# Performance work log

Measured on AMD Instinct MI355X. Metric: run time of the kernel, lower is better.

## Reference

```python
import math
import jax, jax.numpy as jnp
import numpy as np

B, L, D_IN, H, NLAYER, FUT, MDIM = 16, 128, 8, 128, 2, 12, 2

def setup_inputs() -> dict:
    key = jax.random.key(0)
    ks = jax.random.split(key, 16)
    def rn(k, shape, scale=0.05):
        return jax.random.normal(k, shape, jnp.float32) * scale
    return {
        'history': jax.random.normal(ks[0], (B, L, D_IN), jnp.float32),
        'history_mask': jnp.ones((B, L), jnp.float32),
        'Wp': rn(ks[1], (D_IN, H)), 'bp': jnp.zeros((H,), jnp.float32),
        'We1': rn(ks[2], (NLAYER, 4, H)), 'be1': jnp.zeros((NLAYER, H), jnp.float32),
        'We2': rn(ks[3], (NLAYER, H, H)), 'be2': jnp.zeros((NLAYER, H), jnp.float32),
        'Wa1': rn(ks[4], (NLAYER, 3 * H, H)), 'ba1': jnp.zeros((NLAYER, H), jnp.float32),
        'wa2': rn(ks[5], (NLAYER, H)), 'ba2': jnp.zeros((NLAYER,), jnp.float32),
        'Wm1': rn(ks[6], (NLAYER, 2 * H, H)), 'bm1': jnp.zeros((NLAYER, H), jnp.float32),
        'Wm2': rn(ks[7], (NLAYER, H, H)), 'bm2': jnp.zeros((NLAYER, H), jnp.float32),
        'Wo1': rn(ks[8], (NLAYER, 2 * H, H)), 'bo1': jnp.zeros((NLAYER, H), jnp.float32),
        'Wo2': rn(ks[9], (NLAYER, H, H)), 'bo2': jnp.zeros((NLAYER, H), jnp.float32),
        'ln_g': jnp.ones((NLAYER, H), jnp.float32), 'ln_b': jnp.zeros((NLAYER, H), jnp.float32),
        'hg': jnp.ones((D_IN + H,), jnp.float32), 'hb': jnp.zeros((D_IN + H,), jnp.float32),
        'Wh1': rn(ks[10], (D_IN + H, H)), 'bh1': jnp.zeros((H,), jnp.float32),
        'Wh2': rn(ks[11], (H, FUT * MDIM)), 'bh2': jnp.zeros((FUT * MDIM,), jnp.float32),
    }

def _layer_norm(x, g, b):
    mu = jnp.mean(x, -1, keepdims=True)
    var = jnp.mean((x - mu) ** 2, -1, keepdims=True)
    return (x - mu) * jax.lax.rsqrt(var + 1e-5) * g + b

def _forward(history, history_mask, Wp, bp, We1, be1, We2, be2, Wa1, ba1, wa2, ba2,
             Wm1, bm1, Wm2, bm2, Wo1, bo1, Wo2, bo2, ln_g, ln_b, hg, hb, Wh1, bh1, Wh2, bh2):
    valid = history_mask > 0
    vm = valid.astype(jnp.float32)[..., None]
    ts = jnp.cumsum(jnp.maximum(history[..., 5], 0.0), axis=1)
    # edge features [B,L,L,4]: dist, dt/300, same_src, same_step
    lat, lon, src_flag = history[..., 0], history[..., 1], history[..., 6]
    dlat = lat[:, :, None] - lat[:, None, :]
    dlon = lon[:, :, None] - lon[:, None, :]
    dist = jnp.sqrt(dlat * dlat + dlon * dlon + 1e-8)
    dt = jnp.abs(ts[:, :, None] - ts[:, None, :]) / 300.0
    same_src = (src_flag[:, :, None] == src_flag[:, None, :]).astype(jnp.float32)
    same_step = jnp.broadcast_to(jnp.eye(L, dtype=jnp.float32), (B, L, L))
    edge_feat = jnp.stack([dist, dt, same_src, same_step], axis=-1)
    h = (history @ Wp + bp) * vm
    inv = 1.0 / math.sqrt(H)
    for l in range(NLAYER):
        eh = jax.nn.relu(edge_feat @ We1[l] + be1[l]) @ We2[l] + be2[l]  # [B,L,L,H]
        # att MLP on concat([src,dst,edge]) -> split first weight into blocks
        sa = h @ Wa1[l, :H]       # src term, varies over i
        da = h @ Wa1[l, H:2 * H]  # dst term, varies over j
        att_hid = jnp.tanh(sa[:, :, None, :] + da[:, None, :, :] + eh @ Wa1[l, 2 * H:] + ba1[l])
        att = (att_hid @ wa2[l] + ba2[l]) * inv  # [B,L,L]
        att = jnp.where(valid[:, None, :], att, -1e9)  # key invalid
        att = jnp.where(valid[:, :, None], att, -1e9)  # query invalid
        w = jax.nn.softmax(att, axis=-1)
        # msg MLP on concat([src, edge])
        msg = jax.nn.relu((h @ Wm1[l, :H])[:, :, None, :] + eh @ Wm1[l, H:] + bm1[l]) @ Wm2[l] + bm2[l]
        agg = jnp.einsum('bij,bijk->bik', w, msg)
        out = jax.nn.relu(h @ Wo1[l, :H] + agg @ Wo1[l, H:] + bo1[l]) @ Wo2[l] + bo2[l]
        h = _layer_norm(h + out, ln_g[l], ln_b[l]) * vm
    # decoder state: last valid step
    vc = jnp.clip(jnp.sum(history_mask, axis=1).astype(jnp.int32), 1, L)
    last = vc - 1
    bidx = jnp.arange(B)
    ds = jnp.concatenate([history[bidx, last], h[bidx, last]], axis=-1)
    x = _layer_norm(ds, hg, hb)
    pred = (jax.nn.relu(x @ Wh1 + bh1) @ Wh2 + bh2).reshape(B, FUT, MDIM)
    pred = jnp.nan_to_num(pred, nan=0.0, posinf=1e4, neginf=-1e4)
    return pred, h

def reference(history, history_mask, Wp, bp, We1, be1, We2, be2, Wa1, ba1, wa2, ba2,
              Wm1, bm1, Wm2, bm2, Wo1, bo1, Wo2, bo2, ln_g, ln_b, hg, hb, Wh1, bh1, Wh2, bh2):
    return _forward(history, history_mask, Wp, bp, We1, be1, We2, be2, Wa1, ba1, wa2, ba2,
                    Wm1, bm1, Wm2, bm2, Wo1, bo1, Wo2, bo2, ln_g, ln_b, hg, hb, Wh1, bh1, Wh2, bh2)
```

## Files before the change

kernel.cpp:

```cpp
#include <hip/hip_runtime.h>
#include <math.h>

#define BB 16
#define LL 128
#define D_IN 8
#define HH 128
#define NLAYER 2
#define FUT 12
#define MDIM 2

typedef __attribute__((ext_vector_type(8))) __bf16 bf16x8;
typedef __attribute__((ext_vector_type(8))) short short8v;
typedef __attribute__((ext_vector_type(4))) float f32x4;

#define MFMA_B16(A, B, C) __builtin_amdgcn_mfma_f32_16x16x32_bf16(A, B, C, 0, 0, 0)

static __device__ __forceinline__ short f2bf(float f) {
    union { float f; unsigned u; } v; v.f = f;
    unsigned r = v.u + 0x7FFFu + ((v.u >> 16) & 1u);
    return (short)(r >> 16);
}

static __device__ __forceinline__ float tanh_fast(float x) {
    float e = __expf(2.f * x);
    return 1.f - 2.f / (e + 1.f);
}

__global__ __launch_bounds__(LL) void k_ts(const float* __restrict__ hist, float* __restrict__ ts) {
    int b = blockIdx.x, j = threadIdx.x;
    __shared__ float s[LL];
    s[j] = fmaxf(hist[(b * LL + j) * D_IN + 5], 0.f);
    __syncthreads();
    for (int d = 1; d < LL; d <<= 1) {
        float add = (j >= d) ? s[j - d] : 0.f;
        __syncthreads();
        s[j] += add;
        __syncthreads();
    }
    ts[b * LL + j] = s[j];
}

__global__ __launch_bounds__(256) void k_h0(const float* __restrict__ hist, const float* __restrict__ mask,
                                            const float* __restrict__ Wp, const float* __restrict__ bp,
                                            float* __restrict__ h) {
    int idx = blockIdx.x * 256 + threadIdx.x;
    if (idx >= BB * LL * HH) return;
    int k = idx & (HH - 1);
    int bi = idx >> 7;
    const float* hr = hist + (size_t)bi * D_IN;
    float acc = bp[k];
#pragma unroll
    for (int f = 0; f < D_IN; f++) acc += hr[f] * Wp[f * HH + k];
    float vm = mask[bi] > 0.f ? 1.f : 0.f;
    h[idx] = acc * vm;
}

__global__ __launch_bounds__(HH) void k_compose(const float* __restrict__ We2, const float* __restrict__ be2,
                                                const float* __restrict__ Wa1, const float* __restrict__ ba1,
                                                const float* __restrict__ Wm1, const float* __restrict__ bm1,
                                                short* __restrict__ AmT, short* __restrict__ MmT,
                                                float* __restrict__ ca, float* __restrict__ cm) {
    int blk = blockIdx.x;
    int l = blk / (HH + 1);
    int p = blk % (HH + 1);
    int q = threadIdx.x;
    __shared__ float row[HH];
    const float* WaE = Wa1 + (size_t)(l * 3 * HH + 2 * HH) * HH;
    const float* WmE = Wm1 + (size_t)(l * 2 * HH + HH) * HH;
    if (p < HH) {
        row[q] = We2[(size_t)(l * HH + p) * HH + q];
        __syncthreads();
        float a = 0.f, m = 0.f;
        for (int k = 0; k < HH; k++) { float w = row[k]; a += w * WaE[k * HH + q]; m += w * WmE[k * HH + q]; }
        AmT[(size_t)l * HH * HH + q * HH + p] = f2bf(a);
        MmT[(size_t)l * HH * HH + q * HH + p] = f2bf(m);
    } else {
        row[q] = be2[l * HH + q];
        __syncthreads();
        float a = 0.f, m = 0.f;
        for (int k = 0; k < HH; k++) { float w = row[k]; a += w * WaE[k * HH + q]; m += w * WmE[k * HH + q]; }
        ca[l * HH + q] = a + ba1[l * HH + q];
        cm[l * HH + q] = m + bm1[l * HH + q];
    }
}

__global__ __launch_bounds__(256) void k_wconv(const float* __restrict__ Wa1, const float* __restrict__ Wm1,
                                               const float* __restrict__ Wo1, const float* __restrict__ Wm2,
                                               const float* __restrict__ Wo2,
                                               short* __restrict__ WT4, short* __restrict__ WT3) {
    int blk = blockIdx.x;
    int l = blk / 7, m = blk % 7;
    const float* src;
    switch (m) {
        case 0: src = Wa1 + (size_t)(l * 3 * HH) * HH; break;
        case 1: src = Wa1 + (size_t)(l * 3 * HH + HH) * HH; break;
        case 2: src = Wm1 + (size_t)(l * 2 * HH) * HH; break;
        case 3: src = Wo1 + (size_t)(l * 2 * HH) * HH; break;
        case 4: src = Wm2 + (size_t)l * HH * HH; break;
        case 5: src = Wo1 + (size_t)(l * 2 * HH + HH) * HH; break;
        default: src = Wo2 + (size_t)l * HH * HH; break;
    }
    short* dst = (m < 4) ? (WT4 + (size_t)(l * 4 + m) * HH * HH) : (WT3 + (size_t)(l * 3 + (m - 4)) * HH * HH);
    int tid = threadIdx.x;
#pragma unroll 4
    for (int e = 0; e < 64; e++) {
        int idx = e * 256 + tid;
        int c = idx >> 7, k = idx & (HH - 1);
        dst[c * HH + k] = f2bf(src[k * HH + c]);
    }
}

__global__ __launch_bounds__(256) void k_pre(const float* __restrict__ h, const short* __restrict__ WT4,
                                             const float* __restrict__ ca, const float* __restrict__ cm,
                                             float* __restrict__ base_a, float* __restrict__ da,
                                             float* __restrict__ base_m, float* __restrict__ oa, int l) {
    __shared__ __align__(16) short hA[32][136];
    const int tid = threadIdx.x, lane = tid & 63, wv = tid >> 6;
    const int lo = lane & 15, g4 = lane >> 4;
    const int r0 = blockIdx.x * 32;
    {
        int row = tid >> 3, cc = (tid & 7) * 16;
        const float* hr = h + (size_t)(r0 + row) * HH + cc;
        short8v pk;
#pragma unroll
        for (int e = 0; e < 8; e++) pk[e] = f2bf(hr[e]);
        *(short8v*)&hA[row][cc] = pk;
#pragma unroll
        for (int e = 0; e < 8; e++) pk[e] = f2bf(hr[8 + e]);
        *(short8v*)&hA[row][cc + 8] = pk;
    }
    __syncthreads();
    bf16x8 af[2][4];
#pragma unroll
    for (int mt = 0; mt < 2; mt++)
#pragma unroll
        for (int ks = 0; ks < 4; ks++)
            af[mt][ks] = *(const bf16x8*)&hA[mt * 16 + lo][ks * 32 + g4 * 8];
    const short* Wl = WT4 + (size_t)(l * 4 + wv) * HH * HH;
    float* dst;
    const float* bias = nullptr;
    if (wv == 0) { dst = base_a; bias = ca + l * HH; }
    else if (wv == 1) dst = da;
    else if (wv == 2) { dst = base_m; bias = cm + l * HH; }
    else dst = oa;
#pragma unroll
    for (int ct = 0; ct < 8; ct++) {
        int col = ct * 16 + lo;
        bf16x8 Bf[4];
#pragma unroll
        for (int ks = 0; ks < 4; ks++)
            Bf[ks] = *(const bf16x8*)(Wl + (size_t)col * HH + ks * 32 + g4 * 8);
        f32x4 acc[2];
        acc[0] = (f32x4){0.f, 0.f, 0.f, 0.f};
        acc[1] = (f32x4){0.f, 0.f, 0.f, 0.f};
#pragma unroll
        for (int ks = 0; ks < 4; ks++) {
            acc[0] = MFMA_B16(af[0][ks], Bf[ks], acc[0]);
            acc[1] = MFMA_B16(af[1][ks], Bf[ks], acc[1]);
        }
        float bv = bias ? bias[col] : 0.f;
#pragma unroll
        for (int mt = 0; mt < 2; mt++)
#pragma unroll
            for (int rg = 0; rg < 4; rg++)
                dst[(size_t)(r0 + mt * 16 + g4 * 4 + rg) * HH + col] = acc[mt][rg] + bv;
    }
}

__global__ __launch_bounds__(256, 4) void k_attn(
    const float* __restrict__ hist, const float* __restrict__ mask, const float* __restrict__ ts,
    const float* __restrict__ base_a_g, const float* __restrict__ base_m_g, const float* __restrict__ da,
    const short* __restrict__ AmT, const short* __restrict__ MmT,
    const float* __restrict__ wa2, const float* __restrict__ ba2,
    const float* __restrict__ We1, const float* __restrict__ be1,
    float* __restrict__ v_out, int l) {
    __shared__ __align__(16) short t_lds[LL][136];
    __shared__ float bufA[512];
    __shared__ float bufB[128];
    __shared__ float val_s[128], base_a[128], base_m[128], wa2_s[128];

    const int tid = threadIdx.x;
    const int lane = tid & 63;
    const int wv = tid >> 6;
    const int lo = lane & 15, g4 = lane >> 4;
    const int bi = blockIdx.x, b = bi >> 7, i = bi & (LL - 1);

    bf16x8 Bf[2][4];
#pragma unroll
    for (int ct = 0; ct < 2; ct++) {
        int col = wv * 32 + ct * 16 + lo;
#pragma unroll
        for (int ks = 0; ks < 4; ks++)
            Bf[ct][ks] = *(const bf16x8*)(AmT + (size_t)l * HH * HH + col * HH + ks * 32 + g4 * 8);
    }

    const float* We1l = We1 + l * 4 * HH;
    bufA[tid] = We1l[tid];
    bufA[tid + 256] = We1l[tid + 256];
    if (tid < LL) {
        val_s[tid] = mask[b * LL + tid];
        wa2_s[tid] = wa2[l * HH + tid];
        bufB[tid] = be1[l * HH + tid];
        base_a[tid] = base_a_g[(size_t)bi * HH + tid];
        base_m[tid] = base_m_g[(size_t)bi * HH + tid];
    }
    __syncthreads();

    {
        int jj = tid & (LL - 1);
        const float* hri = hist + (size_t)(b * LL + i) * D_IN;
        const float* hrj = hist + (size_t)(b * LL + jj) * D_IN;
        float dlat = hri[0] - hrj[0], dlon = hri[1] - hrj[1];
        float ea = sqrtf(dlat * dlat + dlon * dlon + 1e-8f);
        float eb = fabsf(ts[b * LL + i] - ts[b * LL + jj]) * (1.f / 300.f);
        float ec = (hri[6] == hrj[6]) ? 1.f : 0.f;
        float ed = (jj == i) ? 1.f : 0.f;
#pragma unroll
        for (int pass = 0; pass < 8; pass++) {
            int r0 = ((tid >> 7) + pass * 2) * 8;
            short8v pk;
#pragma unroll
            for (int e = 0; e < 8; e++) {
                int r = r0 + e;
                float v = ea * bufA[r] + eb * bufA[128 + r] + ec * bufA[256 + r] + ed * bufA[384 + r] + bufB[r];
                pk[e] = f2bf(fmaxf(v, 0.f));
            }
            *(short8v*)&t_lds[jj][r0] = pk;
        }
    }

    f32x4 acc[8][2];
    const float* da_b = da + (size_t)(b * LL) * HH;
#pragma unroll
    for (int jt = 0; jt < 8; jt++)
#pragma unroll
        for (int ct = 0; ct < 2; ct++)
#pragma unroll
            for (int rg = 0; rg < 4; rg++)
                acc[jt][ct][rg] = da_b[(size_t)(jt * 16 + g4 * 4 + rg) * HH + wv * 32 + ct * 16 + lo];
    __syncthreads();

#pragma unroll
    for (int ks = 0; ks < 4; ks++) {
#pragma unroll
        for (int jh = 0; jh < 2; jh++) {
            bf16x8 tf[4];
#pragma unroll
            for (int m = 0; m < 4; m++)
                tf[m] = *(const bf16x8*)&t_lds[(jh * 4 + m) * 16 + lo][ks * 32 + g4 * 8];
#pragma unroll
            for (int m = 0; m < 4; m++) {
                acc[jh * 4 + m][0] = MFMA_B16(tf[m], Bf[0][ks], acc[jh * 4 + m][0]);
                acc[jh * 4 + m][1] = MFMA_B16(tf[m], Bf[1][ks], acc[jh * 4 + m][1]);
            }
        }
    }

#pragma unroll
    for (int ct = 0; ct < 2; ct++) {
        int col = wv * 32 + ct * 16 + lo;
#pragma unroll
        for (int ks = 0; ks < 4; ks++)
            Bf[ct][ks] = *(const bf16x8*)(MmT + (size_t)l * HH * HH + col * HH + ks * 32 + g4 * 8);
    }

    {
        int k0 = wv * 32 + lo, k1 = k0 + 16;
        float ba0 = base_a[k0], ba1v = base_a[k1];
        float w0a = wa2_s[k0], w1a = wa2_s[k1];
#pragma unroll
        for (int jt = 0; jt < 8; jt++) {
#pragma unroll
            for (int rg = 0; rg < 4; rg++) {
                float p = tanh_fast(acc[jt][0][rg] + ba0) * w0a + tanh_fast(acc[jt][1][rg] + ba1v) * w1a;
                p += __shfl_xor(p, 1);
                p += __shfl_xor(p, 2);
                p += __shfl_xor(p, 4);
                p += __shfl_xor(p, 8);
                if (lo == 0) bufA[wv * LL + jt * 16 + g4 * 4 + rg] = p;
            }
        }
    }
    __syncthreads();

    float w0, w1;
    {
        const float inv = 0.08838834764831845f;
        float ba2l = ba2[l];
        float vi = val_s[i];
        float a0 = (bufA[lane] + bufA[128 + lane] + bufA[256 + lane] + bufA[384 + lane] + ba2l) * inv;
        float a1 = (bufA[64 + lane] + bufA[192 + lane] + bufA[320 + lane] + bufA[448 + lane] + ba2l) * inv;
        if (!(val_s[lane] > 0.f) || !(vi > 0.f)) a0 = -1e9f;
        if (!(val_s[64 + lane] > 0.f) || !(vi > 0.f)) a1 = -1e9f;
        float m = fmaxf(a0, a1);
#pragma unroll
        for (int d = 1; d < 64; d <<= 1) m = fmaxf(m, __shfl_xor(m, d));
        float e0 = __expf(a0 - m), e1 = __expf(a1 - m);
        float s = e0 + e1;
#pragma unroll
        for (int d = 1; d < 64; d <<= 1) s += __shfl_xor(s, d);
        float rs = 1.f / s;
        w0 = e0 * rs;
        w1 = e1 * rs;
    }

#pragma unroll
    for (int jt = 0; jt < 8; jt++)
#pragma unroll
        for (int ct = 0; ct < 2; ct++)
#pragma unroll
            for (int rg = 0; rg < 4; rg++) acc[jt][ct][rg] = 0.f;
#pragma unroll
    for (int ks = 0; ks < 4; ks++) {
#pragma unroll
        for (int jh = 0; jh < 2; jh++) {
            bf16x8 tf[4];
#pragma unroll
            for (int m = 0; m < 4; m++)
                tf[m] = *(const bf16x8*)&t_lds[(jh * 4 + m) * 16 + lo][ks * 32 + g4 * 8];
#pragma unroll
            for (int m = 0; m < 4; m++) {
                acc[jh * 4 + m][0] = MFMA_B16(tf[m], Bf[0][ks], acc[jh * 4 + m][0]);
                acc[jh * 4 + m][1] = MFMA_B16(tf[m], Bf[1][ks], acc[jh * 4 + m][1]);
            }
        }
    }

    {
        int k0 = wv * 32 + lo;
        float bm0 = base_m[k0], bm1v = base_m[k0 + 16];
        float mac0 = 0.f, mac1 = 0.f;
#pragma unroll
        for (int jt = 0; jt < 8; jt++) {
#pragma unroll
            for (int rg = 0; rg < 4; rg++) {
                int j = jt * 16 + g4 * 4 + rg;
                float wj = (jt < 4) ? __shfl(w0, j) : __shfl(w1, j - 64);
                mac0 += wj * fmaxf(acc[jt][0][rg] + bm0, 0.f);
                mac1 += wj * fmaxf(acc[jt][1][rg] + bm1v, 0.f);
            }
        }
        mac0 += __shfl_xor(mac0, 16);
        mac0 += __shfl_xor(mac0, 32);
        mac1 += __shfl_xor(mac1, 16);
        mac1 += __shfl_xor(mac1, 32);
        if (g4 == 0) {
            v_out[(size_t)bi * HH + wv * 32 + lo] = mac0;
            v_out[(size_t)bi * HH + wv * 32 + 16 + lo] = mac1;
        }
    }
}

__global__ __launch_bounds__(256) void k_post(
    const float* __restrict__ v, const float* __restrict__ oa, const float* __restrict__ h,
    const float* __restrict__ mask, const short* __restrict__ WT3,
    const float* __restrict__ bm2, const float* __restrict__ bo1, const float* __restrict__ bo2,
    const float* __restrict__ ln_g, const float* __restrict__ ln_b,
    float* __restrict__ hout, float* __restrict__ hcopy, int l) {
    __shared__ __align__(16) short xA[32][136];
    __shared__ __align__(16) short iA[32][136];
    __shared__ float red[2][4][32];
    const int tid = threadIdx.x, lane = tid & 63, wv = tid >> 6;
    const int lo = lane & 15, g4 = lane >> 4;
    const int r0 = blockIdx.x * 32;

    float oaR[2][2][4], hR[2][2][4], vmR[2][4];
    float bm2R[2], bo1R[2], bo2R[2], gR[2], bR[2];
#pragma unroll
    for (int ct = 0; ct < 2; ct++) {
        int c = wv * 32 + ct * 16 + lo;
        bm2R[ct] = bm2[l * HH + c];
        bo1R[ct] = bo1[l * HH + c];
        bo2R[ct] = bo2[l * HH + c];
        gR[ct] = ln_g[l * HH + c];
        bR[ct] = ln_b[l * HH + c];
    }
#pragma unroll
    for (int mt = 0; mt < 2; mt++)
#pragma unroll
        for (int rg = 0; rg < 4; rg++) {
            int r = r0 + mt * 16 + g4 * 4 + rg;
            vmR[mt][rg] = mask[r];
#pragma unroll
            for (int ct = 0; ct < 2; ct++) {
                int c = wv * 32 + ct * 16 + lo;
                oaR[mt][ct][rg] = oa[(size_t)r * HH + c];
                hR[mt][ct][rg] = h[(size_t)r * HH + c];
            }
        }

    {
        int row = tid >> 3, cc = (tid & 7) * 16;
        const float* vr = v + (size_t)(r0 + row) * HH + cc;
        short8v pk;
#pragma unroll
        for (int e = 0; e < 8; e++) pk[e] = f2bf(vr[e]);
        *(short8v*)&xA[row][cc] = pk;
#pragma unroll
        for (int e = 0; e < 8; e++) pk[e] = f2bf(vr[8 + e]);
        *(short8v*)&xA[row][cc + 8] = pk;
    }
    __syncthreads();

    bf16x8 af[2][4], Bf[2][4];
    f32x4 acc[2][2];

    {
        const short* W = WT3 + (size_t)(l * 3 + 0) * HH * HH;
#pragma unroll
        for (int mt = 0; mt < 2; mt++)
#pragma unroll
            for (int ks = 0; ks < 4; ks++)
                af[mt][ks] = *(const bf16x8*)&xA[mt * 16 + lo][ks * 32 + g4 * 8];
#pragma unroll
        for (int ct = 0; ct < 2; ct++) {
            int col = wv * 32 + ct * 16 + lo;
#pragma unroll
            for (int ks = 0; ks < 4; ks++)
                Bf[ct][ks] = *(const bf16x8*)(W + (size_t)col * HH + ks * 32 + g4 * 8);
        }
#pragma unroll
        for (int mt = 0; mt < 2; mt++)
#pragma unroll
            for (int ct = 0; ct < 2; ct++) acc[mt][ct] = (f32x4){0.f, 0.f, 0.f, 0.f};
#pragma unroll
        for (int ks = 0; ks < 4; ks++)
#pragma unroll
            for (int mt = 0; mt < 2; mt++) {
                acc[mt][0] = MFMA_B16(af[mt][ks], Bf[0][ks], acc[mt][0]);
                acc[mt][1] = MFMA_B16(af[mt][ks], Bf[1][ks], acc[mt][1]);
            }
#pragma unroll
        for (int mt = 0; mt < 2; mt++)
#pragma unroll
            for (int ct = 0; ct < 2; ct++)
#pragma unroll
                for (int rg = 0; rg < 4; rg++)
                    iA[mt * 16 + g4 * 4 + rg][wv * 32 + ct * 16 + lo] = f2bf(acc[mt][ct][rg] + bm2R[ct]);
    }
    __syncthreads();

    {
        const short* W = WT3 + (size_t)(l * 3 + 1) * HH * HH;
#pragma unroll
        for (int mt = 0; mt < 2; mt++)
#pragma unroll
            for (int ks = 0; ks < 4; ks++)
                af[mt][ks] = *(const bf16x8*)&iA[mt * 16 + lo][ks * 32 + g4 * 8];
#pragma unroll
        for (int ct = 0; ct < 2; ct++) {
            int col = wv * 32 + ct * 16 + lo;
#pragma unroll
            for (int ks = 0; ks < 4; ks++)
                Bf[ct][ks] = *(const bf16x8*)(W + (size_t)col * HH + ks * 32 + g4 * 8);
        }
#pragma unroll
        for (int mt = 0; mt < 2; mt++)
#pragma unroll
            for (int ct = 0; ct < 2; ct++) acc[mt][ct] = (f32x4){0.f, 0.f, 0.f, 0.f};
#pragma unroll
        for (int ks = 0; ks < 4; ks++)
#pragma unroll
            for (int mt = 0; mt < 2; mt++) {
                acc[mt][0] = MFMA_B16(af[mt][ks], Bf[0][ks], acc[mt][0]);
                acc[mt][1] = MFMA_B16(af[mt][ks], Bf[1][ks], acc[mt][1]);
            }
#pragma unroll
        for (int mt = 0; mt < 2; mt++)
#pragma unroll
            for (int ct = 0; ct < 2; ct++)
#pragma unroll
                for (int rg = 0; rg < 4; rg++)
                    xA[mt * 16 + g4 * 4 + rg][wv * 32 + ct * 16 + lo] =
                        f2bf(fmaxf(acc[mt][ct][rg] + oaR[mt][ct][rg] + bo1R[ct], 0.f));
    }
    __syncthreads();

    float y[2][2][4];
    {
        const short* W = WT3 + (size_t)(l * 3 + 2) * HH * HH;
#pragma unroll
        for (int mt = 0; mt < 2; mt++)
#pragma unroll
            for (int ks = 0; ks < 4; ks++)
                af[mt][ks] = *(const bf16x8*)&xA[mt * 16 + lo][ks * 32 + g4 * 8];
#pragma unroll
        for (int ct = 0; ct < 2; ct++) {
            int col = wv * 32 + ct * 16 + lo;
#pragma unroll
            for (int ks = 0; ks < 4; ks++)
                Bf[ct][ks] = *(const bf16x8*)(W + (size_t)col * HH + ks * 32 + g4 * 8);
        }
#pragma unroll
        for (int mt = 0; mt < 2; mt++)
#pragma unroll
            for (int ct = 0; ct < 2; ct++) acc[mt][ct] = (f32x4){0.f, 0.f, 0.f, 0.f};
#pragma unroll
        for (int ks = 0; ks < 4; ks++)
#pragma unroll
            for (int mt = 0; mt < 2; mt++) {
                acc[mt][0] = MFMA_B16(af[mt][ks], Bf[0][ks], acc[mt][0]);
                acc[mt][1] = MFMA_B16(af[mt][ks], Bf[1][ks], acc[mt][1]);
            }
#pragma unroll
        for (int mt = 0; mt < 2; mt++)
#pragma unroll
            for (int ct = 0; ct < 2; ct++)
#pragma unroll
                for (int rg = 0; rg < 4; rg++)
                    y[mt][ct][rg] = acc[mt][ct][rg] + bo2R[ct] + hR[mt][ct][rg];
    }
#pragma unroll
    for (int mt = 0; mt < 2; mt++)
#pragma unroll
        for (int rg = 0; rg < 4; rg++) {
            float s = y[mt][0][rg] + y[mt][1][rg];
            float s2 = y[mt][0][rg] * y[mt][0][rg] + y[mt][1][rg] * y[mt][1][rg];
#pragma unroll
            for (int d = 1; d < 16; d <<= 1) { s += __shfl_xor(s, d); s2 += __shfl_xor(s2, d); }
            if (lo == 0) {
                red[0][wv][mt * 16 + g4 * 4 + rg] = s;
                red[1][wv][mt * 16 + g4 * 4 + rg] = s2;
            }
        }
    __syncthreads();
#pragma unroll
    for (int mt = 0; mt < 2; mt++)
#pragma unroll
        for (int rg = 0; rg < 4; rg++) {
            int rl = mt * 16 + g4 * 4 + rg;
            float mu = (red[0][0][rl] + red[0][1][rl] + red[0][2][rl] + red[0][3][rl]) * (1.f / HH);
            float ex2 = (red[1][0][rl] + red[1][1][rl] + red[1][2][rl] + red[1][3][rl]) * (1.f / HH);
            float var = ex2 - mu * mu;
            float rs = rsqrtf(var + 1e-5f);
            float vm = vmR[mt][rg] > 0.f ? 1.f : 0.f;
            int r = r0 + rl;
#pragma unroll
            for (int ct = 0; ct < 2; ct++) {
                int c = wv * 32 + ct * 16 + lo;
                float hv = ((y[mt][ct][rg] - mu) * rs * gR[ct] + bR[ct]) * vm;
                hout[(size_t)r * HH + c] = hv;
                if (hcopy) hcopy[(size_t)r * HH + c] = hv;
            }
        }
}

__global__ __launch_bounds__(HH) void k_dec(const float* __restrict__ hist, const float* __restrict__ mask,
                                            const float* __restrict__ h, const float* __restrict__ hg,
                                            const float* __restrict__ hb, const float* __restrict__ Wh1,
                                            const float* __restrict__ bh1, const float* __restrict__ Wh2,
                                            const float* __restrict__ bh2, float* __restrict__ out) {
    int b = blockIdx.x, t = threadIdx.x;
    const int N = D_IN + HH;
    __shared__ float red[HH], x_s[D_IN + HH], u_s[HH];
    red[t] = mask[b * LL + t];
    __syncthreads();
    for (int s = 64; s > 0; s >>= 1) { if (t < s) red[t] += red[t + s]; __syncthreads(); }
    int vc = (int)red[0];
    vc = min(max(vc, 1), LL);
    int last = vc - 1;
    __syncthreads();
    if (t < D_IN) x_s[t] = hist[(size_t)(b * LL + last) * D_IN + t];
    x_s[D_IN + t] = h[(size_t)(b * LL + last) * HH + t];
    __syncthreads();
    float ps = 0.f;
    for (int f = t; f < N; f += HH) ps += x_s[f];
    red[t] = ps;
    __syncthreads();
    for (int s = 64; s > 0; s >>= 1) { if (t < s) red[t] += red[t + s]; __syncthreads(); }
    float mu = red[0] / N;
    __syncthreads();
    ps = 0.f;
    for (int f = t; f < N; f += HH) { float d = x_s[f] - mu; ps += d * d; }
    red[t] = ps;
    __syncthreads();
    for (int s = 64; s > 0; s >>= 1) { if (t < s) red[t] += red[t + s]; __syncthreads(); }
    float var = red[0] / N;
    float rs = rsqrtf(var + 1e-5f);
    __syncthreads();
    for (int f = t; f < N; f += HH) x_s[f] = (x_s[f] - mu) * rs * hg[f] + hb[f];
    __syncthreads();
    float acc = bh1[t];
    for (int f = 0; f < N; f++) acc += x_s[f] * Wh1[f * HH + t];
    u_s[t] = fmaxf(acc, 0.f);
    __syncthreads();
    if (t < FUT * MDIM) {
        float o = bh2[t];
        for (int k = 0; k < HH; k++) o += u_s[k] * Wh2[k * FUT * MDIM + t];
        if (isnan(o)) o = 0.f;
        else if (isinf(o)) o = (o > 0.f) ? 1e4f : -1e4f;
        out[b * FUT * MDIM + t] = o;
    }
}

extern "C" void kernel_launch(void* const* d_in, const int* in_sizes, int n_in,
                              void* d_out, int out_size, void* d_ws, size_t ws_size,
                              hipStream_t stream) {
    const float* hist = (const float*)d_in[0];
    const float* mask = (const float*)d_in[1];
    const float* Wp  = (const float*)d_in[2];
    const float* bp  = (const float*)d_in[3];
    const float* We1 = (const float*)d_in[4];
    const float* be1 = (const float*)d_in[5];
    const float* We2 = (const float*)d_in[6];
    const float* be2 = (const float*)d_in[7];
    const float* Wa1 = (const float*)d_in[8];
    const float* ba1 = (const float*)d_in[9];
    const float* wa2 = (const float*)d_in[10];
    const float* ba2 = (const float*)d_in[11];
    const float* Wm1 = (const float*)d_in[12];
    const float* bm1 = (const float*)d_in[13];
    const float* Wm2 = (const float*)d_in[14];
    const float* bm2 = (const float*)d_in[15];
    const float* Wo1 = (const float*)d_in[16];
    const float* bo1 = (const float*)d_in[17];
    const float* Wo2 = (const float*)d_in[18];
    const float* bo2 = (const float*)d_in[19];
    const float* ln_g = (const float*)d_in[20];
    const float* ln_b = (const float*)d_in[21];
    const float* hg  = (const float*)d_in[22];
    const float* hb  = (const float*)d_in[23];
    const float* Wh1 = (const float*)d_in[24];
    const float* bh1 = (const float*)d_in[25];
    const float* Wh2 = (const float*)d_in[26];
    const float* bh2 = (const float*)d_in[27];
    float* out = (float*)d_out;

    float* ws = (float*)d_ws;
    float* ts_w   = ws; ws += BB * LL;
    float* h_w    = ws; ws += BB * LL * HH;
    float* da_w   = ws; ws += BB * LL * HH;
    float* ba_w   = ws; ws += BB * LL * HH;
    float* bm_w   = ws; ws += BB * LL * HH;
    float* oa_w   = ws; ws += BB * LL * HH;
    float* v_w    = ws; ws += BB * LL * HH;
    float* ca_w   = ws; ws += NLAYER * HH;
    float* cm_w   = ws; ws += NLAYER * HH;
    short* AmT_w  = (short*)ws; ws += NLAYER * HH * HH / 2;
    short* MmT_w  = (short*)ws; ws += NLAYER * HH * HH / 2;
    short* WT4_w  = (short*)ws; ws += NLAYER * 4 * HH * HH / 2;
    short* WT3_w  = (short*)ws; ws += NLAYER * 3 * HH * HH / 2;

    k_ts<<<BB, LL, 0, stream>>>(hist, ts_w);
    k_h0<<<(BB * LL * HH + 255) / 256, 256, 0, stream>>>(hist, mask, Wp, bp, h_w);
    k_compose<<<NLAYER * (HH + 1), HH, 0, stream>>>(We2, be2, Wa1, ba1, Wm1, bm1, AmT_w, MmT_w, ca_w, cm_w);
    k_wconv<<<NLAYER * 7, 256, 0, stream>>>(Wa1, Wm1, Wo1, Wm2, Wo2, WT4_w, WT3_w);
    for (int l = 0; l < NLAYER; l++) {
        k_pre<<<BB * LL / 32, 256, 0, stream>>>(h_w, WT4_w, ca_w, cm_w, ba_w, da_w, bm_w, oa_w, l);
        k_attn<<<BB * LL, 256, 0, stream>>>(hist, mask, ts_w, ba_w, bm_w, da_w, AmT_w, MmT_w,
                                            wa2, ba2, We1, be1, v_w, l);
        float* hcopy = (l == NLAYER - 1) ? (out + BB * FUT * MDIM) : nullptr;
        k_post<<<BB * LL / 32, 256, 0, stream>>>(v_w, oa_w, h_w, mask, WT3_w, bm2, bo1, bo2,
                                                 ln_g, ln_b, h_w, hcopy, l);
    }
    k_dec<<<BB, HH, 0, stream>>>(hist, mask, h_w, hg, hb, Wh1, bh1, Wh2, bh2, out);
}
```

Before: 298.4 us.

## Merge setup kernels and fuse next-layer projection into post-layer kernel

Merges the cumsum and input-projection kernels into one, merges weight composition and transposition into one setup kernel, and folds the next layer's pre-projection GEMM into the tail of k_post so the layer-1 k_pre launch disappears. It also drops the occupancy hint on k_attn. The aim is fewer launches and one less global round trip of h. The risks are less parallelism in k_init (16 blocks), a larger k_post, and the oa buffer being read and written within the same kernel, which relies on each block touching only its own rows.

New measurement: 309.1 us. 3.6% more time.

```diff
diff --git a/kernel.cpp b/kernel.cpp
--- a/kernel.cpp
+++ b/kernel.cpp
@@ -26,87 +26,89 @@
     return 1.f - 2.f / (e + 1.f);
 }
 
-__global__ __launch_bounds__(LL) void k_ts(const float* __restrict__ hist, float* __restrict__ ts) {
-    int b = blockIdx.x, j = threadIdx.x;
+__global__ __launch_bounds__(256) void k_init(const float* __restrict__ hist, const float* __restrict__ mask,
+                                              const float* __restrict__ Wp, const float* __restrict__ bp,
+                                              float* __restrict__ ts, float* __restrict__ h) {
+    int b = blockIdx.x, tid = threadIdx.x;
     __shared__ float s[LL];
-    s[j] = fmaxf(hist[(b * LL + j) * D_IN + 5], 0.f);
+    if (tid < LL) s[tid] = fmaxf(hist[(b * LL + tid) * D_IN + 5], 0.f);
     __syncthreads();
     for (int d = 1; d < LL; d <<= 1) {
-        float add = (j >= d) ? s[j - d] : 0.f;
+        float add = (tid < LL && tid >= d) ? s[tid - d] : 0.f;
         __syncthreads();
-        s[j] += add;
+        if (tid < LL) s[tid] += add;
         __syncthreads();
     }
-    ts[b * LL + j] = s[j];
-}
-
-__global__ __launch_bounds__(256) void k_h0(const float* __restrict__ hist, const float* __restrict__ mask,
-                                            const float* __restrict__ Wp, const float* __restrict__ bp,
-                                            float* __restrict__ h) {
-    int idx = blockIdx.x * 256 + threadIdx.x;
-    if (idx >= BB * LL * HH) return;
-    int k = idx & (HH - 1);
-    int bi = idx >> 7;
-    const float* hr = hist + (size_t)bi * D_IN;
-    float acc = bp[k];
-#pragma unroll
-    for (int f = 0; f < D_IN; f++) acc += hr[f] * Wp[f * HH + k];
-    float vm = mask[bi] > 0.f ? 1.f : 0.f;
-    h[idx] = acc * vm;
-}
-
-__global__ __launch_bounds__(HH) void k_compose(const float* __restrict__ We2, const float* __restrict__ be2,
-                                                const float* __restrict__ Wa1, const float* __restrict__ ba1,
-                                                const float* __restrict__ Wm1, const float* __restrict__ bm1,
-                                                short* __restrict__ AmT, short* __restrict__ MmT,
-                                                float* __restrict__ ca, float* __restrict__ cm) {
-    int blk = blockIdx.x;
-    int l = blk / (HH + 1);
-    int p = blk % (HH + 1);
-    int q = threadIdx.x;
+    if (tid < LL) ts[b * LL + tid] = s[tid];
+    int k = tid & (HH - 1);
+    float wp_r[D_IN];
+#pragma unroll
+    for (int f = 0; f < D_IN; f++) wp_r[f] = Wp[f * HH + k];
+    float bpk = bp[k];
+    int jbase = tid >> 7;
+    for (int e = 0; e < 64; e++) {
+        int j = e * 2 + jbase;
+        int bj = b * LL + j;
+        const float* hr = hist + (size_t)bj * D_IN;
+        float acc = bpk;
+#pragma unroll
+        for (int f = 0; f < D_IN; f++) acc += hr[f] * wp_r[f];
+        h[(size_t)bj * HH + k] = acc * (mask[bj] > 0.f ? 1.f : 0.f);
+    }
+}
+
+__global__ __launch_bounds__(HH) void k_setup(const float* __restrict__ We2, const float* __restrict__ be2,
+                                              const float* __restrict__ Wa1, const float* __restrict__ ba1,
+                                              const float* __restrict__ Wm1, const float* __restrict__ bm1,
+                                              const float* __restrict__ Wo1, const float* __restrict__ Wm2,
+                                              const float* __restrict__ Wo2,
+                                              short* __restrict__ AmT, short* __restrict__ MmT,
+                                              float* __restrict__ ca, float* __restrict__ cm,
+                                              short* __restrict__ WT4, short* __restrict__ WT3) {
     __shared__ float row[HH];
-    const float* WaE = Wa1 + (size_t)(l * 3 * HH + 2 * HH) * HH;
-    const float* WmE = Wm1 + (size_t)(l * 2 * HH + HH) * HH;
-    if (p < HH) {
-        row[q] = We2[(size_t)(l * HH + p) * HH + q];
-        __syncthreads();
-        float a = 0.f, m = 0.f;
-        for (int k = 0; k < HH; k++) { float w = row[k]; a += w * WaE[k * HH + q]; m += w * WmE[k * HH + q]; }
-        AmT[(size_t)l * HH * HH + q * HH + p] = f2bf(a);
-        MmT[(size_t)l * HH * HH + q * HH + p] = f2bf(m);
+    int blk = blockIdx.x, q = threadIdx.x;
+    const int NC = NLAYER * (HH + 1);
+    if (blk < NC) {
+        int l = blk / (HH + 1);
+        int p = blk % (HH + 1);
+        const float* WaE = Wa1 + (size_t)(l * 3 * HH + 2 * HH) * HH;
+        const float* WmE = Wm1 + (size_t)(l * 2 * HH + HH) * HH;
+        if (p < HH) {
+            row[q] = We2[(size_t)(l * HH + p) * HH + q];
+            __syncthreads();
+            float a = 0.f, m = 0.f;
+            for (int k = 0; k < HH; k++) { float w = row[k]; a += w * WaE[k * HH + q]; m += w * WmE[k * HH + q]; }
+            AmT[(size_t)l * HH * HH + q * HH + p] = f2bf(a);
+            MmT[(size_t)l * HH * HH + q * HH + p] = f2bf(m);
+        } else {
+            row[q] = be2[l * HH + q];
+            __syncthreads();
+            float a = 0.f, m = 0.f;
+            for (int k = 0; k < HH; k++) { float w = row[k]; a += w * WaE[k * HH + q]; m += w * WmE[k * HH + q]; }
+            ca[l * HH + q] = a + ba1[l * HH + q];
+            cm[l * HH + q] = m + bm1[l * HH + q];
+        }
     } else {
-        row[q] = be2[l * HH + q];
-        __syncthreads();
-        float a = 0.f, m = 0.f;
-        for (int k = 0; k < HH; k++) { float w = row[k]; a += w * WaE[k * HH + q]; m += w * WmE[k * HH + q]; }
-        ca[l * HH + q] = a + ba1[l * HH + q];
-        cm[l * HH + q] = m + bm1[l * HH + q];
-    }
-}
-
-__global__ __launch_bounds__(256) void k_wconv(const float* __restrict__ Wa1, const float* __restrict__ Wm1,
-                                               const float* __restrict__ Wo1, const float* __restrict__ Wm2,
-                                               const float* __restrict__ Wo2,
-                                               short* __restrict__ WT4, short* __restrict__ WT3) {
-    int blk = blockIdx.x;
-    int l = blk / 7, m = blk % 7;
-    const float* src;
-    switch (m) {
-        case 0: src = Wa1 + (size_t)(l * 3 * HH) * HH; break;
-        case 1: src = Wa1 + (size_t)(l * 3 * HH + HH) * HH; break;
-        case 2: src = Wm1 + (size_t)(l * 2 * HH) * HH; break;
-        case 3: src = Wo1 + (size_t)(l * 2 * HH) * HH; break;
-        case 4: src = Wm2 + (size_t)l * HH * HH; break;
-        case 5: src = Wo1 + (size_t)(l * 2 * HH + HH) * HH; break;
-        default: src = Wo2 + (size_t)l * HH * HH; break;
-    }
-    short* dst = (m < 4) ? (WT4 + (size_t)(l * 4 + m) * HH * HH) : (WT3 + (size_t)(l * 3 + (m - 4)) * HH * HH);
-    int tid = threadIdx.x;
+        int m7 = blk - NC;
+        int l = m7 / 7, m = m7 % 7;
+        const float* src;
+        switch (m) {
+            case 0: src = Wa1 + (size_t)(l * 3 * HH) * HH; break;
+            case 1: src = Wa1 + (size_t)(l * 3 * HH + HH) * HH; break;
+            case 2: src = Wm1 + (size_t)(l * 2 * HH) * HH; break;
+            case 3: src = Wo1 + (size_t)(l * 2 * HH) * HH; break;
+            case 4: src = Wm2 + (size_t)l * HH * HH; break;
+            case 5: src = Wo1 + (size_t)(l * 2 * HH + HH) * HH; break;
+            default: src = Wo2 + (size_t)l * HH * HH; break;
+        }
+        short* dst = (m < 4) ? (WT4 + (size_t)(l * 4 + m) * HH * HH)
+                             : (WT3 + (size_t)(l * 3 + (m - 4)) * HH * HH);
 #pragma unroll 4
-    for (int e = 0; e < 64; e++) {
-        int idx = e * 256 + tid;
-        int c = idx >> 7, k = idx & (HH - 1);
-        dst[c * HH + k] = f2bf(src[k * HH + c]);
+        for (int e = 0; e < 128; e++) {
+            int idx = e * 128 + q;
+            int c = idx >> 7, kk = idx & (HH - 1);
+            dst[c * HH + kk] = f2bf(src[kk * HH + c]);
+        }
     }
 }
 
@@ -167,7 +169,7 @@
     }
 }
 
-__global__ __launch_bounds__(256, 4) void k_attn(
+__global__ __launch_bounds__(256) void k_attn(
     const float* __restrict__ hist, const float* __restrict__ mask, const float* __restrict__ ts,
     const float* __restrict__ base_a_g, const float* __restrict__ base_m_g, const float* __restrict__ da,
     const short* __restrict__ AmT, const short* __restrict__ MmT,
@@ -352,11 +354,13 @@
 }
 
 __global__ __launch_bounds__(256) void k_post(
-    const float* __restrict__ v, const float* __restrict__ oa, const float* __restrict__ h,
+    const float* __restrict__ v, const float* __restrict__ oa_in, const float* __restrict__ h,
     const float* __restrict__ mask, const short* __restrict__ WT3,
     const float* __restrict__ bm2, const float* __restrict__ bo1, const float* __restrict__ bo2,
     const float* __restrict__ ln_g, const float* __restrict__ ln_b,
-    float* __restrict__ hout, float* __restrict__ hcopy, int l) {
+    float* __restrict__ hout, float* __restrict__ hcopy, int l,
+    int do_pre, const short* __restrict__ WT4, const float* __restrict__ ca, const float* __restrict__ cm,
+    float* __restrict__ base_a, float* __restrict__ da, float* __restrict__ base_m, float* __restrict__ oa_out) {
     __shared__ __align__(16) short xA[32][136];
     __shared__ __align__(16) short iA[32][136];
     __shared__ float red[2][4][32];
@@ -384,7 +388,7 @@
 #pragma unroll
             for (int ct = 0; ct < 2; ct++) {
                 int c = wv * 32 + ct * 16 + lo;
-                oaR[mt][ct][rg] = oa[(size_t)r * HH + c];
+                oaR[mt][ct][rg] = oa_in[(size_t)r * HH + c];
                 hR[mt][ct][rg] = h[(size_t)r * HH + c];
             }
         }
@@ -465,6 +469,7 @@
                 acc[mt][0] = MFMA_B16(af[mt][ks], Bf[0][ks], acc[mt][0]);
                 acc[mt][1] = MFMA_B16(af[mt][ks], Bf[1][ks], acc[mt][1]);
             }
+        __syncthreads();
 #pragma unroll
         for (int mt = 0; mt < 2; mt++)
 #pragma unroll
@@ -541,8 +546,49 @@
                 float hv = ((y[mt][ct][rg] - mu) * rs * gR[ct] + bR[ct]) * vm;
                 hout[(size_t)r * HH + c] = hv;
                 if (hcopy) hcopy[(size_t)r * HH + c] = hv;
-            }
-        }
+                if (do_pre) xA[rl][c] = f2bf(hv);
+            }
+        }
+
+    if (do_pre) {
+        __syncthreads();
+        bf16x8 af2[2][4];
+#pragma unroll
+        for (int mt = 0; mt < 2; mt++)
+#pragma unroll
+            for (int ks = 0; ks < 4; ks++)
+                af2[mt][ks] = *(const bf16x8*)&xA[mt * 16 + lo][ks * 32 + g4 * 8];
+        int ln = l + 1;
+        const short* Wl = WT4 + (size_t)(ln * 4 + wv) * HH * HH;
+        float* dst;
+        const float* bias = nullptr;
+        if (wv == 0) { dst = base_a; bias = ca + ln * HH; }
+        else if (wv == 1) dst = da;
+        else if (wv == 2) { dst = base_m; bias = cm + ln * HH; }
+        else dst = oa_out;
+#pragma unroll
+        for (int ct = 0; ct < 8; ct++) {
+            int col = ct * 16 + lo;
+            bf16x8 Bf2[4];
+#pragma unroll
+            for (int ks = 0; ks < 4; ks++)
+                Bf2[ks] = *(const bf16x8*)(Wl + (size_t)col * HH + ks * 32 + g4 * 8);
+            f32x4 a2[2];
+            a2[0] = (f32x4){0.f, 0.f, 0.f, 0.f};
+            a2[1] = (f32x4){0.f, 0.f, 0.f, 0.f};
+#pragma unroll
+            for (int ks = 0; ks < 4; ks++) {
+                a2[0] = MFMA_B16(af2[0][ks], Bf2[ks], a2[0]);
+                a2[1] = MFMA_B16(af2[1][ks], Bf2[ks], a2[1]);
+            }
+            float bv = bias ? bias[col] : 0.f;
+#pragma unroll
+            for (int mt = 0; mt < 2; mt++)
+#pragma unroll
+                for (int rg = 0; rg < 4; rg++)
+                    dst[(size_t)(r0 + mt * 16 + g4 * 4 + rg) * HH + col] = a2[mt][rg] + bv;
+        }
+    }
 }
 
 __global__ __launch_bounds__(HH) void k_dec(const float* __restrict__ hist, const float* __restrict__ mask,
@@ -641,17 +687,19 @@
     short* WT4_w  = (short*)ws; ws += NLAYER * 4 * HH * HH / 2;
     short* WT3_w  = (short*)ws; ws += NLAYER * 3 * HH * HH / 2;
 
-    k_ts<<<BB, LL, 0, stream>>>(hist, ts_w);
-    k_h0<<<(BB * LL * HH + 255) / 256, 256, 0, stream>>>(hist, mask, Wp, bp, h_w);
-    k_compose<<<NLAYER * (HH + 1), HH, 0, stream>>>(We2, be2, Wa1, ba1, Wm1, bm1, AmT_w, MmT_w, ca_w, cm_w);
-    k_wconv<<<NLAYER * 7, 256, 0, stream>>>(Wa1, Wm1, Wo1, Wm2, Wo2, WT4_w, WT3_w);
+    k_init<<<BB, 256, 0, stream>>>(hist, mask, Wp, bp, ts_w, h_w);
+    k_setup<<<NLAYER * (HH + 1) + NLAYER * 7, HH, 0, stream>>>(We2, be2, Wa1, ba1, Wm1, bm1,
+                                                               Wo1, Wm2, Wo2, AmT_w, MmT_w, ca_w, cm_w,
+                                                               WT4_w, WT3_w);
+    k_pre<<<BB * LL / 32, 256, 0, stream>>>(h_w, WT4_w, ca_w, cm_w, ba_w, da_w, bm_w, oa_w, 0);
     for (int l = 0; l < NLAYER; l++) {
-        k_pre<<<BB * LL / 32, 256, 0, stream>>>(h_w, WT4_w, ca_w, cm_w, ba_w, da_w, bm_w, oa_w, l);
         k_attn<<<BB * LL, 256, 0, stream>>>(hist, mask, ts_w, ba_w, bm_w, da_w, AmT_w, MmT_w,
                                             wa2, ba2, We1, be1, v_w, l);
+        int do_pre = (l < NLAYER - 1) ? 1 : 0;
         float* hcopy = (l == NLAYER - 1) ? (out + BB * FUT * MDIM) : nullptr;
         k_post<<<BB * LL / 32, 256, 0, stream>>>(v_w, oa_w, h_w, mask, WT3_w, bm2, bo1, bo2,
-                                                 ln_g, ln_b, h_w, hcopy, l);
+                                                 ln_g, ln_b, h_w, hcopy, l,
+                                                 do_pre, WT4_w, ca_w, cm_w, ba_w, da_w, bm_w, oa_w);
     }
     k_dec<<<BB, HH, 0, stream>>>(hist, mask, h_w, hg, hb, Wh1, bh1, Wh2, bh2, out);
 }
```
